# Kernel optimization log

Hardware: AMD Instinct MI355X
Metric: run time of the kernel (lower is better)

The kernel has to match this reference:

```python
import jax, jax.numpy as jnp
import numpy as np
import math

B, T, VOCAB, RANK = 32, 1024, 512, 256


def setup_inputs() -> dict:
    key = jax.random.key(0)
    k1, k2, k3, k4, k5 = jax.random.split(key, 5)
    scale_attn = 1.0 / math.sqrt(VOCAB)
    scale_proj = 1.0 / math.sqrt(RANK)
    return {
        "x": jax.random.normal(k1, (B, T, VOCAB), dtype=jnp.float32),
        "W_attn": jax.random.normal(k2, (VOCAB, 3 * RANK), dtype=jnp.float32) * scale_attn,
        "b_attn": jax.random.normal(k3, (3 * RANK,), dtype=jnp.float32) * 0.01,
        "W_proj": jax.random.normal(k4, (RANK, VOCAB), dtype=jnp.float32) * scale_proj,
        "b_proj": jax.random.normal(k5, (VOCAB,), dtype=jnp.float32) * 0.01,
    }


def reference(x, W_attn, b_attn, W_proj, b_proj):
    # x: [B, T, vocab]
    Bb, Tt, _ = x.shape
    qkv = x @ W_attn + b_attn              # [B, T, 3*rank]
    q, k, v = jnp.split(qkv, 3, axis=-1)   # each [B, T, rank]
    scale = 1.0 / math.sqrt(k.shape[-1])
    att = jnp.einsum('btd,bsd->bts', q, k) * scale  # [B, T, T]
    # causal mask (masked=True)
    mask = jnp.tril(jnp.ones((Tt, Tt), dtype=bool))
    att = jnp.where(mask[None, :, :], att, -jnp.inf)
    att = jax.nn.softmax(att, axis=-1)
    # dropout layers are identity in eval mode (p=0 attn, p=0.1 resid disabled)
    y = jnp.einsum('bts,bsd->btd', att, v)  # [B, T, rank]
    y = y @ W_proj + b_proj                 # [B, T, vocab]
    return jax.nn.gelu(y, approximate=False)
```

## Files before the change

### kernel.cpp

```cpp
#include <hip/hip_runtime.h>
#include <hip/hip_bf16.h>
#include <math.h>

typedef __bf16 bf16;
typedef __attribute__((ext_vector_type(8))) __bf16 bf16x8;
typedef __attribute__((ext_vector_type(4))) __bf16 bf16x4;
typedef __attribute__((ext_vector_type(4))) float f32x4;

#define MFMA16(a, b, c) __builtin_amdgcn_mfma_f32_16x16x32_bf16((a), (b), (c), 0, 0, 0)


__global__ __launch_bounds__(256) void cvt_wattn(const float* __restrict__ w,
                                                 bf16* __restrict__ wt) {
  int o = blockIdx.x * 256 + threadIdx.x;
  int n = o >> 9, kk = o & 511;
  wt[o] = (bf16)w[kk * 768 + n];
}

__global__ __launch_bounds__(256) void cvt_wproj(const float* __restrict__ w,
                                                 bf16* __restrict__ wt) {
  int o = blockIdx.x * 256 + threadIdx.x;
  int n = o >> 8, kk = o & 255;
  wt[o] = (bf16)w[kk * 512 + n];
}

__global__ __launch_bounds__(256) void gemm_qkv(
    const float* __restrict__ x, const bf16* __restrict__ WT,
    const float* __restrict__ b_attn,
    bf16* __restrict__ qo, bf16* __restrict__ ko, bf16* __restrict__ vo) {
  __shared__ __attribute__((aligned(16))) bf16 As[128][40];
  __shared__ __attribute__((aligned(16))) bf16 Bs[128][40];
  const int tid = threadIdx.x;
  const int id = blockIdx.x;
  const int xcd = id & 7;
  const int rest = id >> 3;
  const int bmL = rest / 6;
  const int bn = (rest % 6) * 128;
  const int bm = (xcd * 32 + bmL) * 128;
  const int lane = tid & 63, wid = tid >> 6;
  const int l15 = lane & 15, lg = lane >> 4;
  const int wm = (wid >> 1) * 64, wn = (wid & 1) * 64;

  f32x4 acc[4][4] = {};

  const int srow = tid >> 1;
  const int scol = (tid & 1) * 16;
  const float* xp = x + (size_t)(bm + srow) * 512 + scol;
  const bf16* wp = WT + (size_t)(bn + srow) * 512 + scol;

  bf16x8 ha[2], hb[2];
  {
    f32x4 f0 = *(const f32x4*)(xp);
    f32x4 f1 = *(const f32x4*)(xp + 4);
    f32x4 f2 = *(const f32x4*)(xp + 8);
    f32x4 f3 = *(const f32x4*)(xp + 12);
#pragma unroll
    for (int e = 0; e < 4; ++e) {
      ha[0][e] = (bf16)f0[e]; ha[0][e + 4] = (bf16)f1[e];
      ha[1][e] = (bf16)f2[e]; ha[1][e + 4] = (bf16)f3[e];
    }
    hb[0] = *(const bf16x8*)(wp);
    hb[1] = *(const bf16x8*)(wp + 8);
  }

  for (int kt = 0; kt < 16; ++kt) {
    __syncthreads();
    *(bf16x8*)&As[srow][scol] = ha[0];
    *(bf16x8*)&As[srow][scol + 8] = ha[1];
    *(bf16x8*)&Bs[srow][scol] = hb[0];
    *(bf16x8*)&Bs[srow][scol + 8] = hb[1];
    __syncthreads();
    if (kt < 15) {
      f32x4 f0 = *(const f32x4*)(xp + (kt + 1) * 32);
      f32x4 f1 = *(const f32x4*)(xp + (kt + 1) * 32 + 4);
      f32x4 f2 = *(const f32x4*)(xp + (kt + 1) * 32 + 8);
      f32x4 f3 = *(const f32x4*)(xp + (kt + 1) * 32 + 12);
#pragma unroll
      for (int e = 0; e < 4; ++e) {
        ha[0][e] = (bf16)f0[e]; ha[0][e + 4] = (bf16)f1[e];
        ha[1][e] = (bf16)f2[e]; ha[1][e + 4] = (bf16)f3[e];
      }
      hb[0] = *(const bf16x8*)(wp + (kt + 1) * 32);
      hb[1] = *(const bf16x8*)(wp + (kt + 1) * 32 + 8);
    }
    bf16x8 af[4], bfr[4];
#pragma unroll
    for (int mi = 0; mi < 4; ++mi)
      af[mi] = *(const bf16x8*)&As[wm + mi * 16 + l15][lg * 8];
#pragma unroll
    for (int ni = 0; ni < 4; ++ni)
      bfr[ni] = *(const bf16x8*)&Bs[wn + ni * 16 + l15][lg * 8];
    __builtin_amdgcn_s_setprio(1);
#pragma unroll
    for (int mi = 0; mi < 4; ++mi)
#pragma unroll
      for (int ni = 0; ni < 4; ++ni)
        acc[mi][ni] = MFMA16(af[mi], bfr[ni], acc[mi][ni]);
    __builtin_amdgcn_s_setprio(0);
  }

#pragma unroll
  for (int ni = 0; ni < 4; ++ni) {
    int gc = bn + wn + ni * 16 + l15;
    float bias = b_attn[gc];
    int seg = gc >> 8;
    int cc = gc & 255;
    bf16* op = (seg == 0) ? qo : ((seg == 1) ? ko : vo);
#pragma unroll
    for (int mi = 0; mi < 4; ++mi) {
      int gr = bm + wm + mi * 16 + lg * 4;
#pragma unroll
      for (int r = 0; r < 4; ++r) {
        float v = acc[mi][ni][r] + bias;
        op[(size_t)(gr + r) * 256 + cc] = (bf16)v;
      }
    }
  }
}

__global__ __launch_bounds__(256) void transpose_v(const bf16* __restrict__ v,
                                                   bf16* __restrict__ vt) {
  __shared__ bf16 tile[32][33];
  const int b = blockIdx.z;
  const int t0 = blockIdx.x * 32;
  const int d0 = blockIdx.y * 32;
  const int tid = threadIdx.x;
  const int r = tid >> 3, c4 = (tid & 7) * 4;
  bf16x4 in = *(const bf16x4*)(v + (size_t)(b * 1024 + t0 + r) * 256 + d0 + c4);
  tile[r][c4] = in[0]; tile[r][c4 + 1] = in[1];
  tile[r][c4 + 2] = in[2]; tile[r][c4 + 3] = in[3];
  __syncthreads();
  bf16x4 o;
  o[0] = tile[c4][r]; o[1] = tile[c4 + 1][r];
  o[2] = tile[c4 + 2][r]; o[3] = tile[c4 + 3][r];
  *(bf16x4*)(vt + (size_t)(b * 256 + d0 + r) * 1024 + t0 + c4) = o;
}

__global__ __launch_bounds__(512) void attn_fwd(
    const bf16* __restrict__ q, const bf16* __restrict__ k,
    const bf16* __restrict__ vt, bf16* __restrict__ y) {
  __shared__ __attribute__((aligned(16))) bf16 Ks[64][264];
  __shared__ __attribute__((aligned(16))) bf16 Vt[256][72];
  __shared__ __attribute__((aligned(16))) bf16 Ps[8][16][72];
  const int tid = threadIdx.x, lane = tid & 63, wid = tid >> 6;
  const int l15 = lane & 15, lg = lane >> 4;

  const int id = blockIdx.x;
  const int xcd = id & 7;
  const int rest = id >> 3;
  const int qt = rest & 7;
  const int bg = rest >> 3;
  const int b = xcd + 8 * bg;
  const int q0 = qt * 128 + wid * 16;

  bf16x8 qf[8];
  {
    const bf16* qp = q + (size_t)(b * 1024 + q0 + l15) * 256 + lg * 8;
#pragma unroll
    for (int d = 0; d < 8; ++d) qf[d] = *(const bf16x8*)(qp + d * 32);
  }
  f32x4 o[16] = {};
  float m_st = -1e30f;
  float l_st = 0.f;

  const bf16* kbase = k + (size_t)b * 1024 * 256;
  const bf16* vtbase = vt + (size_t)b * 256 * 1024;
  const int ksr = tid >> 5, ksc = (tid & 31) * 8;
  const int vsr = tid >> 3, vsc = (tid & 7) * 8;

  const int ntiles = 2 * qt + 2;

  bf16x8 kreg[4], vreg[4];
#pragma unroll
  for (int i = 0; i < 4; ++i)
    kreg[i] = *(const bf16x8*)(kbase + (size_t)(ksr + i * 16) * 256 + ksc);
#pragma unroll
  for (int i = 0; i < 4; ++i)
    vreg[i] = *(const bf16x8*)(vtbase + (size_t)(vsr + i * 64) * 1024 + vsc);

  for (int tt = 0; tt < ntiles; ++tt) {
    const int kv0 = tt * 64;
    __syncthreads();
#pragma unroll
    for (int i = 0; i < 4; ++i)
      *(bf16x8*)&Ks[ksr + i * 16][ksc] = kreg[i];
#pragma unroll
    for (int i = 0; i < 4; ++i)
      *(bf16x8*)&Vt[vsr + i * 64][vsc] = vreg[i];
    __syncthreads();
    if (tt + 1 < ntiles) {
      const bf16* kp = kbase + (size_t)(kv0 + 64 + ksr) * 256 + ksc;
      const bf16* vp = vtbase + (size_t)vsr * 1024 + kv0 + 64 + vsc;
#pragma unroll
      for (int i = 0; i < 4; ++i)
        kreg[i] = *(const bf16x8*)(kp + (size_t)i * 16 * 256);
#pragma unroll
      for (int i = 0; i < 4; ++i)
        vreg[i] = *(const bf16x8*)(vp + (size_t)i * 64 * 1024);
    }

    f32x4 st[4] = {};
    __builtin_amdgcn_s_setprio(1);
#pragma unroll
    for (int nf = 0; nf < 4; ++nf)
#pragma unroll
      for (int dc = 0; dc < 8; ++dc) {
        bf16x8 kb = *(const bf16x8*)&Ks[nf * 16 + l15][dc * 32 + lg * 8];
        st[nf] = MFMA16(kb, qf[dc], st[nf]);
      }
    __builtin_amdgcn_s_setprio(0);

    const int qg = q0 + l15;
    float tmax = -1e30f;
#pragma unroll
    for (int nf = 0; nf < 4; ++nf)
#pragma unroll
      for (int r = 0; r < 4; ++r) {
        int sg = kv0 + nf * 16 + lg * 4 + r;
        float v = st[nf][r] * 0.0625f;
        v = (sg > qg) ? -1e30f : v;
        st[nf][r] = v;
        tmax = fmaxf(tmax, v);
      }
    tmax = fmaxf(tmax, __shfl_xor(tmax, 16, 64));
    tmax = fmaxf(tmax, __shfl_xor(tmax, 32, 64));

    if (!__all(tmax <= m_st + 8.f)) {
      float mnew = fmaxf(m_st, tmax);
      float corr = __expf(m_st - mnew);
      m_st = mnew;
      l_st *= corr;
      float corrT[4];
#pragma unroll
      for (int r = 0; r < 4; ++r) corrT[r] = __shfl(corr, lg * 4 + r, 64);
#pragma unroll
      for (int df = 0; df < 16; ++df)
#pragma unroll
        for (int r = 0; r < 4; ++r) o[df][r] *= corrT[r];
    }

    float rsum = 0.f;
#pragma unroll
    for (int nf = 0; nf < 4; ++nf) {
      bf16x4 pk;
#pragma unroll
      for (int r = 0; r < 4; ++r) {
        float p = __expf(st[nf][r] - m_st);
        rsum += p;
        pk[r] = (bf16)p;
      }
      *(bf16x4*)&Ps[wid][l15][nf * 16 + lg * 4] = pk;
    }
    rsum += __shfl_xor(rsum, 16, 64);
    rsum += __shfl_xor(rsum, 32, 64);
    l_st += rsum;

    bf16x8 pa0 = *(const bf16x8*)&Ps[wid][l15][lg * 8];
    bf16x8 pa1 = *(const bf16x8*)&Ps[wid][l15][32 + lg * 8];
    __builtin_amdgcn_s_setprio(1);
#pragma unroll
    for (int df = 0; df < 16; ++df) {
      bf16x8 vb0 = *(const bf16x8*)&Vt[df * 16 + l15][lg * 8];
      bf16x8 vb1 = *(const bf16x8*)&Vt[df * 16 + l15][32 + lg * 8];
      o[df] = MFMA16(pa0, vb0, o[df]);
      o[df] = MFMA16(pa1, vb1, o[df]);
    }
    __builtin_amdgcn_s_setprio(0);
  }

  float lT[4];
#pragma unroll
  for (int r = 0; r < 4; ++r) lT[r] = __shfl(l_st, lg * 4 + r, 64);
  const size_t ybase = (size_t)(b * 1024 + q0 + lg * 4) * 256 + l15;
#pragma unroll
  for (int r = 0; r < 4; ++r) {
    float inv = 1.f / lT[r];
#pragma unroll
    for (int df = 0; df < 16; ++df)
      y[ybase + (size_t)r * 256 + df * 16] = (bf16)(o[df][r] * inv);
  }
}

__global__ __launch_bounds__(256) void gemm_proj(
    const bf16* __restrict__ y, const bf16* __restrict__ WT,
    const float* __restrict__ b_proj, float* __restrict__ out) {
  __shared__ __attribute__((aligned(16))) bf16 As[128][40];
  __shared__ __attribute__((aligned(16))) bf16 Bs[128][40];
  const int tid = threadIdx.x;
  const int bn = blockIdx.x * 128;
  const int bm = blockIdx.y * 128;
  const int lane = tid & 63, wid = tid >> 6;
  const int l15 = lane & 15, lg = lane >> 4;
  const int wm = (wid >> 1) * 64, wn = (wid & 1) * 64;
  f32x4 acc[4][4] = {};
  const int srow = tid >> 1, scol = (tid & 1) * 16;
  const bf16* yp = y + (size_t)(bm + srow) * 256 + scol;
  const bf16* wp = WT + (size_t)(bn + srow) * 256 + scol;
  for (int kt = 0; kt < 8; ++kt) {
    bf16x8 a0 = *(const bf16x8*)(yp + kt * 32);
    bf16x8 a1 = *(const bf16x8*)(yp + kt * 32 + 8);
    bf16x8 b0 = *(const bf16x8*)(wp + kt * 32);
    bf16x8 b1 = *(const bf16x8*)(wp + kt * 32 + 8);
    *(bf16x8*)&As[srow][scol] = a0;  *(bf16x8*)&As[srow][scol + 8] = a1;
    *(bf16x8*)&Bs[srow][scol] = b0;  *(bf16x8*)&Bs[srow][scol + 8] = b1;
    __syncthreads();
    bf16x8 af[4], bfr[4];
#pragma unroll
    for (int mi = 0; mi < 4; ++mi)
      af[mi] = *(const bf16x8*)&As[wm + mi * 16 + l15][lg * 8];
#pragma unroll
    for (int ni = 0; ni < 4; ++ni)
      bfr[ni] = *(const bf16x8*)&Bs[wn + ni * 16 + l15][lg * 8];
#pragma unroll
    for (int mi = 0; mi < 4; ++mi)
#pragma unroll
      for (int ni = 0; ni < 4; ++ni)
        acc[mi][ni] = MFMA16(af[mi], bfr[ni], acc[mi][ni]);
    __syncthreads();
  }
#pragma unroll
  for (int ni = 0; ni < 4; ++ni) {
    int gc = bn + wn + ni * 16 + l15;
    float bias = b_proj[gc];
#pragma unroll
    for (int mi = 0; mi < 4; ++mi) {
      int gr = bm + wm + mi * 16 + lg * 4;
#pragma unroll
      for (int r = 0; r < 4; ++r) {
        float v = acc[mi][ni][r] + bias;
        float g = 0.5f * v * (1.0f + erff(v * 0.70710678118654752f));
        out[(size_t)(gr + r) * 512 + gc] = g;
      }
    }
  }
}

extern "C" void kernel_launch(void* const* d_in, const int* in_sizes, int n_in,
                              void* d_out, int out_size, void* d_ws, size_t ws_size,
                              hipStream_t stream) {
  const float* x      = (const float*)d_in[0];
  const float* W_attn = (const float*)d_in[1];
  const float* b_attn = (const float*)d_in[2];
  const float* W_proj = (const float*)d_in[3];
  const float* b_proj = (const float*)d_in[4];
  float* out = (float*)d_out;
  char* ws = (char*)d_ws;

  const size_t SZ = 16777216;
  bf16* WT1 = (bf16*)(ws);
  bf16* WT2 = (bf16*)(ws + 786432);
  bf16* qb  = (bf16*)(ws + 1048576);
  bf16* kb  = (bf16*)(ws + 1048576 + SZ);
  bf16* vb  = (bf16*)(ws + 1048576 + 2 * SZ);
  bf16* vtb = (bf16*)(ws + 1048576 + 3 * SZ);
  bf16* yb  = vb;

  cvt_wattn<<<dim3(1536), dim3(256), 0, stream>>>(W_attn, WT1);
  cvt_wproj<<<dim3(512), dim3(256), 0, stream>>>(W_proj, WT2);
  gemm_qkv<<<dim3(1536), dim3(256), 0, stream>>>(x, WT1, b_attn, qb, kb, vb);
  transpose_v<<<dim3(32, 8, 32), dim3(256), 0, stream>>>(vb, vtb);
  attn_fwd<<<dim3(256), dim3(512), 0, stream>>>(qb, kb, vtb, yb);
  gemm_proj<<<dim3(4, 256), dim3(256), 0, stream>>>(yb, WT2, b_proj, out);
}
```

Measured before the change: 152.5 us.

## Transpose MFMA outputs for vector stores, prefetch and remap proj GEMM, tanh GELU

```diff
diff --git a/kernel.cpp b/kernel.cpp
--- a/kernel.cpp
+++ b/kernel.cpp
@@ -95,25 +95,24 @@
     for (int mi = 0; mi < 4; ++mi)
 #pragma unroll
       for (int ni = 0; ni < 4; ++ni)
-        acc[mi][ni] = MFMA16(af[mi], bfr[ni], acc[mi][ni]);
+        acc[mi][ni] = MFMA16(bfr[ni], af[mi], acc[mi][ni]);
     __builtin_amdgcn_s_setprio(0);
   }
 
 #pragma unroll
   for (int ni = 0; ni < 4; ++ni) {
-    int gc = bn + wn + ni * 16 + l15;
-    float bias = b_attn[gc];
-    int seg = gc >> 8;
-    int cc = gc & 255;
+    int gc0 = bn + wn + ni * 16 + lg * 4;
+    f32x4 bias = *(const f32x4*)(b_attn + gc0);
+    int seg = gc0 >> 8;
+    int cc = gc0 & 255;
     bf16* op = (seg == 0) ? qo : ((seg == 1) ? ko : vo);
 #pragma unroll
     for (int mi = 0; mi < 4; ++mi) {
-      int gr = bm + wm + mi * 16 + lg * 4;
-#pragma unroll
-      for (int r = 0; r < 4; ++r) {
-        float v = acc[mi][ni][r] + bias;
-        op[(size_t)(gr + r) * 256 + cc] = (bf16)v;
-      }
+      int gr = bm + wm + mi * 16 + l15;
+      bf16x4 pk;
+#pragma unroll
+      for (int r = 0; r < 4; ++r) pk[r] = (bf16)(acc[mi][ni][r] + bias[r]);
+      *(bf16x4*)(op + (size_t)gr * 256 + cc) = pk;
     }
   }
 }
@@ -230,13 +229,10 @@
       float corr = __expf(m_st - mnew);
       m_st = mnew;
       l_st *= corr;
-      float corrT[4];
-#pragma unroll
-      for (int r = 0; r < 4; ++r) corrT[r] = __shfl(corr, lg * 4 + r, 64);
 #pragma unroll
       for (int df = 0; df < 16; ++df)
 #pragma unroll
-        for (int r = 0; r < 4; ++r) o[df][r] *= corrT[r];
+        for (int r = 0; r < 4; ++r) o[df][r] *= corr;
     }
 
     float rsum = 0.f;
@@ -262,22 +258,20 @@
     for (int df = 0; df < 16; ++df) {
       bf16x8 vb0 = *(const bf16x8*)&Vt[df * 16 + l15][lg * 8];
       bf16x8 vb1 = *(const bf16x8*)&Vt[df * 16 + l15][32 + lg * 8];
-      o[df] = MFMA16(pa0, vb0, o[df]);
-      o[df] = MFMA16(pa1, vb1, o[df]);
+      o[df] = MFMA16(vb0, pa0, o[df]);
+      o[df] = MFMA16(vb1, pa1, o[df]);
     }
     __builtin_amdgcn_s_setprio(0);
   }
 
-  float lT[4];
-#pragma unroll
-  for (int r = 0; r < 4; ++r) lT[r] = __shfl(l_st, lg * 4 + r, 64);
-  const size_t ybase = (size_t)(b * 1024 + q0 + lg * 4) * 256 + l15;
-#pragma unroll
-  for (int r = 0; r < 4; ++r) {
-    float inv = 1.f / lT[r];
-#pragma unroll
-    for (int df = 0; df < 16; ++df)
-      y[ybase + (size_t)r * 256 + df * 16] = (bf16)(o[df][r] * inv);
+  float inv = 1.f / l_st;
+  bf16* yp = y + (size_t)(b * 1024 + q0 + l15) * 256 + lg * 4;
+#pragma unroll
+  for (int df = 0; df < 16; ++df) {
+    bf16x4 pk;
+#pragma unroll
+    for (int r = 0; r < 4; ++r) pk[r] = (bf16)(o[df][r] * inv);
+    *(bf16x4*)(yp + df * 16) = pk;
   }
 }
 
@@ -287,23 +281,38 @@
   __shared__ __attribute__((aligned(16))) bf16 As[128][40];
   __shared__ __attribute__((aligned(16))) bf16 Bs[128][40];
   const int tid = threadIdx.x;
-  const int bn = blockIdx.x * 128;
-  const int bm = blockIdx.y * 128;
+  const int id = blockIdx.x;
+  const int xcd = id & 7;
+  const int rest = id >> 3;
+  const int bmL = rest >> 2;
+  const int bn = (rest & 3) * 128;
+  const int bm = (xcd * 32 + bmL) * 128;
   const int lane = tid & 63, wid = tid >> 6;
   const int l15 = lane & 15, lg = lane >> 4;
   const int wm = (wid >> 1) * 64, wn = (wid & 1) * 64;
   f32x4 acc[4][4] = {};
+
   const int srow = tid >> 1, scol = (tid & 1) * 16;
   const bf16* yp = y + (size_t)(bm + srow) * 256 + scol;
   const bf16* wp = WT + (size_t)(bn + srow) * 256 + scol;
+
+  bf16x8 ha[2], hb[2];
+  ha[0] = *(const bf16x8*)(yp);
+  ha[1] = *(const bf16x8*)(yp + 8);
+  hb[0] = *(const bf16x8*)(wp);
+  hb[1] = *(const bf16x8*)(wp + 8);
+
   for (int kt = 0; kt < 8; ++kt) {
-    bf16x8 a0 = *(const bf16x8*)(yp + kt * 32);
-    bf16x8 a1 = *(const bf16x8*)(yp + kt * 32 + 8);
-    bf16x8 b0 = *(const bf16x8*)(wp + kt * 32);
-    bf16x8 b1 = *(const bf16x8*)(wp + kt * 32 + 8);
-    *(bf16x8*)&As[srow][scol] = a0;  *(bf16x8*)&As[srow][scol + 8] = a1;
-    *(bf16x8*)&Bs[srow][scol] = b0;  *(bf16x8*)&Bs[srow][scol + 8] = b1;
-    __syncthreads();
+    __syncthreads();
+    *(bf16x8*)&As[srow][scol] = ha[0];  *(bf16x8*)&As[srow][scol + 8] = ha[1];
+    *(bf16x8*)&Bs[srow][scol] = hb[0];  *(bf16x8*)&Bs[srow][scol + 8] = hb[1];
+    __syncthreads();
+    if (kt < 7) {
+      ha[0] = *(const bf16x8*)(yp + (kt + 1) * 32);
+      ha[1] = *(const bf16x8*)(yp + (kt + 1) * 32 + 8);
+      hb[0] = *(const bf16x8*)(wp + (kt + 1) * 32);
+      hb[1] = *(const bf16x8*)(wp + (kt + 1) * 32 + 8);
+    }
     bf16x8 af[4], bfr[4];
 #pragma unroll
     for (int mi = 0; mi < 4; ++mi)
@@ -311,26 +320,32 @@
 #pragma unroll
     for (int ni = 0; ni < 4; ++ni)
       bfr[ni] = *(const bf16x8*)&Bs[wn + ni * 16 + l15][lg * 8];
+    __builtin_amdgcn_s_setprio(1);
 #pragma unroll
     for (int mi = 0; mi < 4; ++mi)
 #pragma unroll
       for (int ni = 0; ni < 4; ++ni)
-        acc[mi][ni] = MFMA16(af[mi], bfr[ni], acc[mi][ni]);
-    __syncthreads();
-  }
+        acc[mi][ni] = MFMA16(bfr[ni], af[mi], acc[mi][ni]);
+    __builtin_amdgcn_s_setprio(0);
+  }
+
 #pragma unroll
   for (int ni = 0; ni < 4; ++ni) {
-    int gc = bn + wn + ni * 16 + l15;
-    float bias = b_proj[gc];
+    int gc0 = bn + wn + ni * 16 + lg * 4;
+    f32x4 bias = *(const f32x4*)(b_proj + gc0);
 #pragma unroll
     for (int mi = 0; mi < 4; ++mi) {
-      int gr = bm + wm + mi * 16 + lg * 4;
+      int gr = bm + wm + mi * 16 + l15;
+      f32x4 g;
 #pragma unroll
       for (int r = 0; r < 4; ++r) {
-        float v = acc[mi][ni][r] + bias;
-        float g = 0.5f * v * (1.0f + erff(v * 0.70710678118654752f));
-        out[(size_t)(gr + r) * 512 + gc] = g;
-      }
+        float v = acc[mi][ni][r] + bias[r];
+        float z = 1.5957691216f * (v + 0.044715f * v * v * v);
+        float t = __expf(z);
+        float th = 1.f - 2.f / (t + 1.f);
+        g[r] = 0.5f * v * (1.f + th);
+      }
+      *(f32x4*)(out + (size_t)gr * 512 + gc0) = g;
     }
   }
 }
@@ -360,5 +375,5 @@
   gemm_qkv<<<dim3(1536), dim3(256), 0, stream>>>(x, WT1, b_attn, qb, kb, vb);
   transpose_v<<<dim3(32, 8, 32), dim3(256), 0, stream>>>(vb, vtb);
   attn_fwd<<<dim3(256), dim3(512), 0, stream>>>(qb, kb, vtb, yb);
-  gemm_proj<<<dim3(4, 256), dim3(256), 0, stream>>>(yb, WT2, b_proj, out);
-}
+  gemm_proj<<<dim3(1024), dim3(256), 0, stream>>>(yb, WT2, b_proj, out);
+}
```

Measured after the change: 153.6 us. Within noise of the previous version (+0.8%).
